# Kernel tuning notes

Hardware: AMD Instinct MI355X
Metric: run time of the kernel (lower is better)

## Reference

```python
import jax, jax.numpy as jnp
from jax import lax
import numpy as np

TAU = 2.0
V_TH = 0.5
SG_ALPHA = 4.0  # spikingjelly default Sigmoid surrogate alpha
POOL = 4
INH_DELAY = 1


@jax.custom_vjp
def heaviside(x):
    return (x >= 0.0).astype(x.dtype)

def _heaviside_fwd(x):
    return heaviside(x), x

def _heaviside_bwd(x, g):
    s = jax.nn.sigmoid(SG_ALPHA * x)
    return (g * SG_ALPHA * s * (1.0 - s),)

heaviside.defvjp(_heaviside_fwd, _heaviside_bwd)


def _gaussian_kernel(size, sigma):
    coords = jnp.arange(size, dtype=jnp.float32) - size // 2
    g = jnp.exp(-coords ** 2 / (2.0 * sigma ** 2))
    k = jnp.outer(g, g)
    return k / k.sum()


def setup_inputs():
    key = jax.random.key(0)
    T, B, H, W = 100, 16, 260, 346
    x = jax.random.uniform(key, (T, B, 2, H, W), dtype=jnp.float32)
    # exc_conv init: channel 0 -> +1.0, channel 1 -> -0.3
    exc_w = jnp.concatenate([jnp.ones((1, 1, 3, 3), jnp.float32),
                             jnp.full((1, 1, 3, 3), -0.3, jnp.float32)], axis=1)
    # inh_conv init: negated Gaussian (size 7, sigma 1.5)
    inh_w = (-_gaussian_kernel(7, 1.5)).reshape(1, 1, 7, 7)
    h, w = H // POOL, W // POOL  # 65, 86
    dcmd_w = jnp.ones((1, 1, h, w), jnp.float32) / (h * w)
    return {"x": x, "exc_w": exc_w, "inh_w": inh_w, "dcmd_w": dcmd_w}


def _conv2d_same(x, w):
    return lax.conv_general_dilated(x, w, window_strides=(1, 1), padding="SAME",
                                    dimension_numbers=("NCHW", "OIHW", "NCHW"))


def reference(x, exc_w, inh_w, dcmd_w):
    T, B, C, H, W = x.shape
    h, w = H // POOL, W // POOL
    # AvgPool2d(4): kernel=stride=4, implicitly crops to multiples of 4
    xp = x.reshape(T * B, C, H, W)[:, :, :h * POOL, :w * POOL]
    p = xp.reshape(T * B, C, h, POOL, w, POOL).mean(axis=(3, 5))
    exc = jax.nn.relu(_conv2d_same(p, exc_w))            # (T*B,1,h,w)
    exc = exc.reshape(T, B, 1, h, w)
    pad = jnp.zeros((INH_DELAY, B, 1, h, w), exc.dtype)
    exc_delayed = jnp.concatenate([pad, lax.stop_gradient(exc[:-INH_DELAY])], axis=0)
    inh = _conv2d_same(exc_delayed.reshape(T * B, 1, h, w), inh_w).reshape(T, B, 1, h, w)
    lgmd_in = exc + inh

    # LIF recurrence (decay_input=True, v_reset=0 hard reset, detach_reset=True)
    def step(v, xt):
        v = v + (xt - v) / TAU
        s = heaviside(v - V_TH)
        v = v * (1.0 - lax.stop_gradient(s))
        return v, s

    v0 = jnp.zeros((B, 1, h, w), x.dtype)
    _, spikes = lax.scan(step, v0, lgmd_in)              # (T,B,1,h,w)

    dcmd = (spikes * dcmd_w).sum(axis=(-1, -2, -3))      # (T,B)
    net_exc = jnp.clip(lgmd_in, 0.0).mean(axis=(-1, -2, -3))  # (T,B)
    return dcmd, spikes, net_exc
```

## Files before the change

kernel.cpp:

```cpp
#include <hip/hip_runtime.h>
#include <hip/hip_bf16.h>

#define T_STEPS 100
#define BATCH   16
#define H_IN    260
#define W_IN    346
#define H_P     65
#define W_P     86
#define HW      (H_P * W_P)
#define NPIX    (BATCH * HW)
#define NIMG    (T_STEPS * BATCH)
#define CHW_IN  (2 * H_IN * W_IN)

__global__ __launch_bounds__(256) void pool_exc_f64(const float* __restrict__ x,
                                                    const float* __restrict__ ew,
                                                    double* __restrict__ exc) {
    const int n   = blockIdx.z;
    const int ti0 = blockIdx.y * 32;
    const int tj0 = blockIdx.x * 32;

    __shared__ double p[2][34][35];
    __shared__ double wsm[18];

    const int tid = threadIdx.x;
    if (tid < 18) wsm[tid] = (double)ew[tid];

    const float* xb = x + (size_t)n * CHW_IN;

    for (int idx = tid; idx < 2 * 34 * 34; idx += 256) {
        const int c  = idx / (34 * 34);
        const int r  = idx % (34 * 34);
        const int ri = r / 34;
        const int rj = r % 34;
        const int pi = ti0 - 1 + ri;
        const int pj = tj0 - 1 + rj;
        double v = 0.0;
        if (pi >= 0 && pi < H_P && pj >= 0 && pj < W_P) {
            const float* base = xb + (size_t)c * (H_IN * W_IN) + (4 * pi) * W_IN + 4 * pj;
            double s = 0.0;
            #pragma unroll
            for (int di = 0; di < 4; ++di) {
                const float2 a = *reinterpret_cast<const float2*>(base + di * W_IN);
                const float2 b = *reinterpret_cast<const float2*>(base + di * W_IN + 2);
                s += (double)a.x + (double)a.y + (double)b.x + (double)b.y;
            }
            v = s * 0.0625;
        }
        p[c][ri][rj] = v;
    }
    __syncthreads();

    const int tx  = tid & 31;
    const int ty0 = tid >> 5;
    #pragma unroll
    for (int q = 0; q < 4; ++q) {
        const int ly = ty0 + q * 8;
        const int i  = ti0 + ly;
        const int j  = tj0 + tx;
        if (i < H_P && j < W_P) {
            double acc = 0.0;
            #pragma unroll
            for (int c = 0; c < 2; ++c)
                #pragma unroll
                for (int ky = 0; ky < 3; ++ky)
                    #pragma unroll
                    for (int kx = 0; kx < 3; ++kx)
                        acc += p[c][ly + ky][tx + kx] * wsm[c * 9 + ky * 3 + kx];
            exc[(size_t)n * HW + i * W_P + j] = (acc > 0.0) ? acc : 0.0;
        }
    }
}

__global__ void init_acc(double* __restrict__ acc) {
    const int n = blockIdx.x * 256 + threadIdx.x;
    if (n < 2 * NIMG) acc[n] = 0.0;
}

__global__ __launch_bounds__(256) void lif_fused(const double* __restrict__ exc,
                                                 const float* __restrict__ iw,
                                                 const float* __restrict__ dw,
                                                 float* __restrict__ spikes,
                                                 double* __restrict__ accd,
                                                 double* __restrict__ accn) {
    const int b = blockIdx.y;
    const int p = blockIdx.x * 256 + threadIdx.x;
    const bool valid = (p < HW);
    const int pc = valid ? p : 0;
    const int i  = pc / W_P;
    const int j  = pc % W_P;

    __shared__ double wsm[49];
    __shared__ double sd[4], sn[4];
    if (threadIdx.x < 49) wsm[threadIdx.x] = (double)iw[threadIdx.x];
    __syncthreads();

    const double wd = valid ? (double)dw[pc] : 0.0;
    double v = 0.0;

    for (int t = 0; t < T_STEPS; ++t) {
        double inh = 0.0;
        if (t > 0 && valid) {
            const double* ep = exc + (size_t)((t - 1) * BATCH + b) * HW;
            #pragma unroll
            for (int dy = 0; dy < 7; ++dy) {
                const int ii = i + dy - 3;
                if ((unsigned)ii < (unsigned)H_P) {
                    const double* row = ep + ii * W_P;
                    #pragma unroll
                    for (int dx = 0; dx < 7; ++dx) {
                        const int jj = j + dx - 3;
                        const double val = ((unsigned)jj < (unsigned)W_P) ? row[jj] : 0.0;
                        inh += val * wsm[dy * 7 + dx];
                    }
                }
            }
        }
        const double ecur = valid ? exc[(size_t)(t * BATCH + b) * HW + pc] : 0.0;
        const double lg   = ecur + inh;

        v = v + (lg - v) * 0.5;
        const double s = (v >= 0.5) ? 1.0 : 0.0;
        v = (s != 0.0) ? 0.0 : v;

        if (valid) spikes[(size_t)t * NPIX + b * HW + pc] = (float)s;

        double pd = s * wd;
        double pn = (lg > 0.0) ? lg : 0.0;
        #pragma unroll
        for (int off = 32; off > 0; off >>= 1) {
            pd += __shfl_down(pd, off);
            pn += __shfl_down(pn, off);
        }
        const int wv = threadIdx.x >> 6;
        if ((threadIdx.x & 63) == 0) { sd[wv] = pd; sn[wv] = pn; }
        __syncthreads();
        if (threadIdx.x == 0) {
            atomicAdd(&accd[t * BATCH + b], sd[0] + sd[1] + sd[2] + sd[3]);
            atomicAdd(&accn[t * BATCH + b], sn[0] + sn[1] + sn[2] + sn[3]);
        }
        __syncthreads();
    }
}

__global__ void finalize(const double* __restrict__ accd,
                         const double* __restrict__ accn,
                         float* __restrict__ dcmd,
                         float* __restrict__ ne) {
    const int n = blockIdx.x * 256 + threadIdx.x;
    if (n < NIMG) {
        dcmd[n] = (float)accd[n];
        ne[n]   = (float)(accn[n] / (double)HW);
    }
}

extern "C" void kernel_launch(void* const* d_in, const int* in_sizes, int n_in,
                              void* d_out, int out_size, void* d_ws, size_t ws_size,
                              hipStream_t stream) {
    const float* x  = (const float*)d_in[0];
    const float* ew = (const float*)d_in[1];
    const float* iw = (const float*)d_in[2];
    const float* dw = (const float*)d_in[3];

    float* out    = (float*)d_out;
    float* dcmd   = out;
    float* spikes = out + NIMG;
    float* ne     = out + NIMG + (size_t)T_STEPS * NPIX;

    double* exc  = (double*)d_ws;
    double* accd = exc + (size_t)T_STEPS * NPIX;
    double* accn = accd + NIMG;

    dim3 gA((W_P + 31) / 32, (H_P + 31) / 32, NIMG);
    pool_exc_f64<<<gA, 256, 0, stream>>>(x, ew, exc);

    init_acc<<<(2 * NIMG + 255) / 256, 256, 0, stream>>>(accd);

    dim3 gC((HW + 255) / 256, BATCH);
    lif_fused<<<gC, 256, 0, stream>>>(exc, iw, dw, spikes, accd, accn);

    finalize<<<(NIMG + 255) / 256, 256, 0, stream>>>(accd, accn, dcmd, ne);
}
```

Baseline: 1.922 ms.

## Split inhibitory conv out of serial LIF scan into fully parallel tiled kernel

The 7x7 inhibitory convolution and the net-excitation reduction move out of the time-serial LIF loop into a new kernel that runs in parallel over all T*B images, using shared-memory tiles with halo. The LIF scan then only streams a precomputed lgmd buffer and drops its block-level syncthreads, using per-wavefront atomics instead. The serial critical path previously ran on only 22x16 blocks, so this exposes much more parallelism. In exchange it adds an extra double-precision intermediate buffer write and read plus one more launch.

New measurement: 1.664 ms. -13.4%, faster.

```diff
diff --git a/kernel.cpp b/kernel.cpp
--- a/kernel.cpp
+++ b/kernel.cpp
@@ -76,69 +76,96 @@
     if (n < 2 * NIMG) acc[n] = 0.0;
 }
 
-__global__ __launch_bounds__(256) void lif_fused(const double* __restrict__ exc,
-                                                 const float* __restrict__ iw,
-                                                 const float* __restrict__ dw,
-                                                 float* __restrict__ spikes,
-                                                 double* __restrict__ accd,
-                                                 double* __restrict__ accn) {
+__global__ __launch_bounds__(256) void inh_lgmd(const double* __restrict__ exc,
+                                                const float* __restrict__ iw,
+                                                double* __restrict__ lgmd,
+                                                double* __restrict__ accn) {
+    const int n   = blockIdx.z;
+    const int t   = n / BATCH;
+    const int ti0 = blockIdx.y * 32;
+    const int tj0 = blockIdx.x * 32;
+
+    __shared__ double e[38][39];
+    __shared__ double wsm[49];
+    __shared__ double sred[4];
+
+    const int tid = threadIdx.x;
+    if (tid < 49) wsm[tid] = (double)iw[tid];
+
+    const double* ep = exc + (size_t)(n - BATCH) * HW;
+    for (int idx = tid; idx < 38 * 38; idx += 256) {
+        const int ri = idx / 38;
+        const int rj = idx % 38;
+        const int ii = ti0 - 3 + ri;
+        const int jj = tj0 - 3 + rj;
+        double v = 0.0;
+        if (t > 0 && (unsigned)ii < (unsigned)H_P && (unsigned)jj < (unsigned)W_P)
+            v = ep[ii * W_P + jj];
+        e[ri][rj] = v;
+    }
+    __syncthreads();
+
+    const double* ec = exc  + (size_t)n * HW;
+    double*       lp = lgmd + (size_t)n * HW;
+
+    const int tx  = tid & 31;
+    const int ty0 = tid >> 5;
+    double psum = 0.0;
+    #pragma unroll
+    for (int q = 0; q < 4; ++q) {
+        const int ly = ty0 + q * 8;
+        const int i  = ti0 + ly;
+        const int j  = tj0 + tx;
+        if (i < H_P && j < W_P) {
+            double acc = 0.0;
+            #pragma unroll
+            for (int ky = 0; ky < 7; ++ky)
+                #pragma unroll
+                for (int kx = 0; kx < 7; ++kx)
+                    acc += e[ly + ky][tx + kx] * wsm[ky * 7 + kx];
+            const double lg = ec[i * W_P + j] + acc;
+            lp[i * W_P + j] = lg;
+            psum += (lg > 0.0) ? lg : 0.0;
+        }
+    }
+
+    #pragma unroll
+    for (int off = 32; off > 0; off >>= 1) psum += __shfl_down(psum, off);
+    if ((tid & 63) == 0) sred[tid >> 6] = psum;
+    __syncthreads();
+    if (tid == 0) atomicAdd(&accn[n], sred[0] + sred[1] + sred[2] + sred[3]);
+}
+
+__global__ __launch_bounds__(256) void lif_scan(const double* __restrict__ lgmd,
+                                                const float* __restrict__ dw,
+                                                float* __restrict__ spikes,
+                                                double* __restrict__ accd) {
     const int b = blockIdx.y;
     const int p = blockIdx.x * 256 + threadIdx.x;
     const bool valid = (p < HW);
     const int pc = valid ? p : 0;
-    const int i  = pc / W_P;
-    const int j  = pc % W_P;
-
-    __shared__ double wsm[49];
-    __shared__ double sd[4], sn[4];
-    if (threadIdx.x < 49) wsm[threadIdx.x] = (double)iw[threadIdx.x];
-    __syncthreads();
 
     const double wd = valid ? (double)dw[pc] : 0.0;
+    const size_t stride = (size_t)BATCH * HW;
+    const double* lp = lgmd   + (size_t)b * HW + pc;
+    float*        sp = spikes + (size_t)b * HW + pc;
+
     double v = 0.0;
-
+    #pragma unroll 2
     for (int t = 0; t < T_STEPS; ++t) {
-        double inh = 0.0;
-        if (t > 0 && valid) {
-            const double* ep = exc + (size_t)((t - 1) * BATCH + b) * HW;
-            #pragma unroll
-            for (int dy = 0; dy < 7; ++dy) {
-                const int ii = i + dy - 3;
-                if ((unsigned)ii < (unsigned)H_P) {
-                    const double* row = ep + ii * W_P;
-                    #pragma unroll
-                    for (int dx = 0; dx < 7; ++dx) {
-                        const int jj = j + dx - 3;
-                        const double val = ((unsigned)jj < (unsigned)W_P) ? row[jj] : 0.0;
-                        inh += val * wsm[dy * 7 + dx];
-                    }
-                }
-            }
-        }
-        const double ecur = valid ? exc[(size_t)(t * BATCH + b) * HW + pc] : 0.0;
-        const double lg   = ecur + inh;
+        const double lgraw = lp[(size_t)t * stride];
+        const double lg = valid ? lgraw : 0.0;
 
         v = v + (lg - v) * 0.5;
         const double s = (v >= 0.5) ? 1.0 : 0.0;
         v = (s != 0.0) ? 0.0 : v;
 
-        if (valid) spikes[(size_t)t * NPIX + b * HW + pc] = (float)s;
+        if (valid) sp[(size_t)t * stride] = (float)s;
 
         double pd = s * wd;
-        double pn = (lg > 0.0) ? lg : 0.0;
         #pragma unroll
-        for (int off = 32; off > 0; off >>= 1) {
-            pd += __shfl_down(pd, off);
-            pn += __shfl_down(pn, off);
-        }
-        const int wv = threadIdx.x >> 6;
-        if ((threadIdx.x & 63) == 0) { sd[wv] = pd; sn[wv] = pn; }
-        __syncthreads();
-        if (threadIdx.x == 0) {
-            atomicAdd(&accd[t * BATCH + b], sd[0] + sd[1] + sd[2] + sd[3]);
-            atomicAdd(&accn[t * BATCH + b], sn[0] + sn[1] + sn[2] + sn[3]);
-        }
-        __syncthreads();
+        for (int off = 32; off > 0; off >>= 1) pd += __shfl_down(pd, off);
+        if ((threadIdx.x & 63) == 0) atomicAdd(&accd[t * BATCH + b], pd);
     }
 }
 
@@ -167,7 +194,8 @@
     float* ne     = out + NIMG + (size_t)T_STEPS * NPIX;
 
     double* exc  = (double*)d_ws;
-    double* accd = exc + (size_t)T_STEPS * NPIX;
+    double* lgmd = exc  + (size_t)T_STEPS * NPIX;
+    double* accd = lgmd + (size_t)T_STEPS * NPIX;
     double* accn = accd + NIMG;
 
     dim3 gA((W_P + 31) / 32, (H_P + 31) / 32, NIMG);
@@ -175,8 +203,11 @@
 
     init_acc<<<(2 * NIMG + 255) / 256, 256, 0, stream>>>(accd);
 
+    dim3 gB((W_P + 31) / 32, (H_P + 31) / 32, NIMG);
+    inh_lgmd<<<gB, 256, 0, stream>>>(exc, iw, lgmd, accn);
+
     dim3 gC((HW + 255) / 256, BATCH);
-    lif_fused<<<gC, 256, 0, stream>>>(exc, iw, dw, spikes, accd, accn);
+    lif_scan<<<gC, 256, 0, stream>>>(lgmd, dw, spikes, accd);
 
     finalize<<<(NIMG + 255) / 256, 256, 0, stream>>>(accd, accn, dcmd, ne);
 }
```
